# Kernel optimization log

Measured on AMD Instinct MI355X. Metric: run time of the kernel, lower is better.

## Reference

```python
import jax, jax.numpy as jnp
import numpy as np

D_MODEL = 1024
EPS = 1e-6

def setup_inputs() -> dict:
    key = jax.random.key(0)
    ks = jax.random.split(key, 13)
    B, T, S, E = 4, 2048, 2048, D_MODEL
    s = 1.0 / np.sqrt(E)
    return {
        "query": jax.random.normal(ks[0], (B, T, E), jnp.float32),
        "key": jax.random.normal(ks[1], (B, S, E), jnp.float32),
        "value": jax.random.normal(ks[2], (B, S, E), jnp.float32),
        "Wq": jax.random.normal(ks[3], (E, E), jnp.float32) * s,
        "bq": jax.random.normal(ks[4], (E,), jnp.float32) * 0.01,
        "Wk": jax.random.normal(ks[5], (E, E), jnp.float32) * s,
        "bk": jax.random.normal(ks[6], (E,), jnp.float32) * 0.01,
        "Wv": jax.random.normal(ks[7], (E, E), jnp.float32) * s,
        "bv": jax.random.normal(ks[8], (E,), jnp.float32) * 0.01,
        "Wo": jax.random.normal(ks[9], (E, E), jnp.float32) * s,
        "bo": jax.random.normal(ks[10], (E,), jnp.float32) * 0.01,
        "gamma": jnp.ones((E,), jnp.float32),
        "beta": jnp.zeros((E,), jnp.float32),
    }

def reference(query, key, value, Wq, bq, Wk, bk, Wv, bv, Wo, bo, gamma, beta):
    # Note: despite the name, the original never splits heads; attention is
    # over the full d_model with scale 1/sqrt(d_model). Dropout = eval identity.
    residual = query
    q = jnp.einsum('bte,fe->btf', query, Wq) + bq   # nn.Linear: x @ W.T + b
    k = jnp.einsum('bse,fe->bsf', key, Wk) + bk
    v = jnp.einsum('bse,fe->bsf', value, Wv) + bv
    scores = jnp.einsum('bte,bse->bts', q, k) / jnp.sqrt(jnp.float32(D_MODEL))
    attn = jax.nn.softmax(scores, axis=-1)          # (B, T, S)
    ctx = jnp.einsum('bts,bse->bte', attn, v)
    out = jnp.einsum('bte,fe->btf', ctx, Wo) + bo
    out = out + residual
    mu = jnp.mean(out, axis=-1, keepdims=True)
    var = jnp.mean(jnp.square(out - mu), axis=-1, keepdims=True)
    return (out - mu) * jax.lax.rsqrt(var + EPS) * gamma + beta
```

## Files before the change

### kernel.cpp

```cpp
#include <hip/hip_runtime.h>
#include <hip/hip_bf16.h>

typedef __bf16 bf16_t;
typedef __bf16 bf16x4 __attribute__((ext_vector_type(4)));
typedef __bf16 bf16x8 __attribute__((ext_vector_type(8)));
typedef float f32x16 __attribute__((ext_vector_type(16)));

#define E_DIM 1024
#define SEQ   2048
#define NBATCH 4

__global__ __launch_bounds__(256) void k_castw(
    const float* __restrict__ wq, const float* __restrict__ wk,
    const float* __restrict__ wv, const float* __restrict__ wo,
    bf16_t* __restrict__ wqb, bf16_t* __restrict__ wkb,
    bf16_t* __restrict__ wvb, bf16_t* __restrict__ wob) {
  const int b = blockIdx.x;
  const int w = b >> 9, r = b & 511;
  const float* s = (w == 0) ? wq : (w == 1) ? wk : (w == 2) ? wv : wo;
  bf16_t* d = (w == 0) ? wqb : (w == 1) ? wkb : (w == 2) ? wvb : wob;
  const long i = (long)r * 2048 + threadIdx.x * 8;
  const float4 a = *(const float4*)(s + i);
  const float4 c = *(const float4*)(s + i + 4);
  bf16x8 o;
  o[0] = (bf16_t)a.x; o[1] = (bf16_t)a.y; o[2] = (bf16_t)a.z; o[3] = (bf16_t)a.w;
  o[4] = (bf16_t)c.x; o[5] = (bf16_t)c.y; o[6] = (bf16_t)c.z; o[7] = (bf16_t)c.w;
  *(bf16x8*)(d + i) = o;
}

template <int OUTMODE, bool RS, bool AF32>
__global__ __launch_bounds__(256, RS ? 2 : 3) void k_g7(
    const void* __restrict__ Av, int lda, long sA,
    const bf16_t* __restrict__ B, int ldb, long sB,
    void* __restrict__ Cv, int ldc, long sC,
    int K, float scale, const float* __restrict__ bias,
    const float* __restrict__ residual, int GM, int GN) {
  constexpr int ABYTES = AF32 ? 32768 : 16384;
  __shared__ __align__(16) char smem[ABYTES + 16384];

  const int tid  = threadIdx.x;
  const int lane = tid & 63;
  const int wid  = tid >> 6;
  const int wm   = wid >> 1, wn = wid & 1;
  const int hi   = lane >> 5;
  const int l31  = lane & 31;

  const int nwg  = gridDim.x;
  const int orig = blockIdx.x;
  const int wg   = (orig & 7) * (nwg >> 3) + (orig >> 3);
  const int zz   = wg / (GM * GN);
  const int rm   = wg - zz * (GM * GN);
  const int bm   = rm / GN;
  const int bn   = rm - bm * GN;
  const int brow = bm * 128;
  const int bcol = bn * 128;

#define GLL(gaddr, ldsoff)                                                       \
  __builtin_amdgcn_global_load_lds(                                             \
      (const __attribute__((address_space(1))) void*)(gaddr),                   \
      (__attribute__((address_space(3))) void*)(smem + (ldsoff)), 16, 0, 0)

  const float*  A32s = AF32 ? (const float*)Av + zz * sA +
                              (long)(brow + (tid >> 4)) * lda +
                              (((tid & 15) ^ ((tid >> 4) & 15)) << 2)
                            : nullptr;
  const bf16_t* A16s = AF32 ? nullptr
                            : (const bf16_t*)Av + zz * sA +
                              (long)(brow + (tid >> 3)) * lda +
                              (((tid & 7) ^ ((tid >> 3) & 7)) << 3);
  const bf16_t* Bs   = B + zz * sB + (long)(bcol + (tid >> 3)) * ldb +
                       (((tid & 7) ^ ((tid >> 3) & 7)) << 3);
  const int ldsw = wid << 10;

  auto stage = [&](int t) {
    const long koff = (long)t * 64;
    if constexpr (AF32) {
#pragma unroll
      for (int s = 0; s < 8; ++s)
        GLL(A32s + (long)(s * 16) * lda + koff, s * 4096 + ldsw);
    } else {
#pragma unroll
      for (int s = 0; s < 4; ++s)
        GLL(A16s + (long)(s * 32) * lda + koff, s * 4096 + ldsw);
    }
#pragma unroll
    for (int s = 0; s < 4; ++s)
      GLL(Bs + (long)(s * 32) * ldb + koff, ABYTES + s * 4096 + ldsw);
  };

  auto ldA = [&](int kk, int ra) -> bf16x8 {
    if constexpr (AF32) {
      const int b = kk * 64 + (hi << 5);
      const int sw = (ra & 15) << 4;
      const float4 f0 = *(const float4*)(smem + ra * 256 + (b ^ sw));
      const float4 f1 = *(const float4*)(smem + ra * 256 + ((b + 16) ^ sw));
      bf16x8 r;
      r[0] = (bf16_t)f0.x; r[1] = (bf16_t)f0.y; r[2] = (bf16_t)f0.z; r[3] = (bf16_t)f0.w;
      r[4] = (bf16_t)f1.x; r[5] = (bf16_t)f1.y; r[6] = (bf16_t)f1.z; r[7] = (bf16_t)f1.w;
      return r;
    } else {
      const int b = kk * 32 + (hi << 4);
      return *(const bf16x8*)(smem + ra * 128 + (b ^ ((ra & 7) << 4)));
    }
  };
  auto ldB = [&](int kk, int rb) -> bf16x8 {
    const int b = kk * 32 + (hi << 4);
    return *(const bf16x8*)(smem + ABYTES + rb * 128 + (b ^ ((rb & 7) << 4)));
  };

  f32x16 acc00 = {}, acc01 = {}, acc10 = {}, acc11 = {};
  f32x16 rs0 = {}, rs1 = {};
  bf16x8 vones;
#pragma unroll
  for (int i = 0; i < 8; ++i) vones[i] = (bf16_t)1.0f;

  const int ra = wm * 64 + l31;
  const int rb = wn * 64 + l31;
  const int NT = K >> 6;

  for (int t = 0; t < NT; ++t) {
    stage(t);
    __syncthreads();
#pragma unroll
    for (int k = 0; k < 4; ++k) {
      bf16x8 a0 = ldA(k, ra), a1 = ldA(k, ra + 32);
      bf16x8 b0 = ldB(k, rb), b1 = ldB(k, rb + 32);
      acc00 = __builtin_amdgcn_mfma_f32_32x32x16_bf16(a0, b0, acc00, 0, 0, 0);
      acc01 = __builtin_amdgcn_mfma_f32_32x32x16_bf16(a0, b1, acc01, 0, 0, 0);
      acc10 = __builtin_amdgcn_mfma_f32_32x32x16_bf16(a1, b0, acc10, 0, 0, 0);
      acc11 = __builtin_amdgcn_mfma_f32_32x32x16_bf16(a1, b1, acc11, 0, 0, 0);
      if constexpr (RS) {
        rs0 = __builtin_amdgcn_mfma_f32_32x32x16_bf16(a0, vones, rs0, 0, 0, 0);
        rs1 = __builtin_amdgcn_mfma_f32_32x32x16_bf16(a1, vones, rs1, 0, 0, 0);
      }
    }
    __syncthreads();
  }

  float inv0[16], inv1[16];
  if constexpr (RS) {
#pragma unroll
    for (int i = 0; i < 16; ++i) { inv0[i] = 1.0f / rs0[i]; inv1[i] = 1.0f / rs1[i]; }
  }
  const int colb = bcol + wn * 64 + l31;
  const int rowb = brow + wm * 64 + (hi << 2);
#pragma unroll
  for (int mf = 0; mf < 2; ++mf) {
#pragma unroll
    for (int nf = 0; nf < 2; ++nf) {
      const f32x16 av = (mf == 0) ? (nf == 0 ? acc00 : acc01) : (nf == 0 ? acc10 : acc11);
      const int colg = colb + nf * 32;
      float bval = 0.0f;
      if constexpr (OUTMODE != 3) bval = bias ? bias[colg] : 0.0f;
#pragma unroll
      for (int g = 0; g < 4; ++g) {
        const int r0 = rowb + mf * 32 + g * 8;
        if constexpr (OUTMODE == 2) {
          bf16x4 pk;
#pragma unroll
          for (int j = 0; j < 4; ++j) pk[j] = (bf16_t)(av[g * 4 + j] * scale + bval);
          const long bb = (long)(r0 >> 11);
          const int ss = r0 & (SEQ - 1);
          *(bf16x4*)((bf16_t*)Cv + bb * ((long)E_DIM * SEQ) + (long)colg * SEQ + ss) = pk;
        } else {
#pragma unroll
          for (int j = 0; j < 4; ++j) {
            const int r = r0 + j;
            float v;
            if constexpr (OUTMODE == 3) v = __expf(av[g * 4 + j] * scale);
            else v = av[g * 4 + j] * scale + bval;
            if constexpr (RS) v *= (mf == 0 ? inv0[g * 4 + j] : inv1[g * 4 + j]);
            if (OUTMODE == 0 && residual) v += residual[(long)r * ldc + colg];
            const long idx = (long)zz * sC + (long)r * ldc + colg;
            if constexpr (OUTMODE == 0) ((float*)Cv)[idx] = v;
            else ((bf16_t*)Cv)[idx] = (bf16_t)v;
          }
        }
      }
    }
  }
#undef GLL
}

__global__ __launch_bounds__(256) void k_layernorm(float* __restrict__ out,
                                                   const float* __restrict__ gamma,
                                                   const float* __restrict__ beta) {
  const long row = blockIdx.x;
  float* rp = out + row * 1024;
  const int t = threadIdx.x;
  const float4 v = *(const float4*)(rp + t * 4);
  float s = v.x + v.y + v.z + v.w;
#pragma unroll
  for (int o = 32; o; o >>= 1) s += __shfl_xor(s, o);
  __shared__ float red1[4], red2[4];
  const int lane = t & 63, w = t >> 6;
  if (lane == 0) red1[w] = s;
  __syncthreads();
  const float mu = (red1[0] + red1[1] + red1[2] + red1[3]) * (1.0f / 1024.0f);
  const float d0 = v.x - mu, d1 = v.y - mu, d2 = v.z - mu, d3 = v.w - mu;
  float ss = d0 * d0 + d1 * d1 + d2 * d2 + d3 * d3;
#pragma unroll
  for (int o = 32; o; o >>= 1) ss += __shfl_xor(ss, o);
  if (lane == 0) red2[w] = ss;
  __syncthreads();
  const float var = (red2[0] + red2[1] + red2[2] + red2[3]) * (1.0f / 1024.0f);
  const float rsq = rsqrtf(var + 1e-6f);
  const float4 g = *(const float4*)(gamma + t * 4);
  const float4 b = *(const float4*)(beta + t * 4);
  float4 o;
  o.x = d0 * rsq * g.x + b.x;
  o.y = d1 * rsq * g.y + b.y;
  o.z = d2 * rsq * g.z + b.z;
  o.w = d3 * rsq * g.w + b.w;
  *(float4*)(rp + t * 4) = o;
}

extern "C" void kernel_launch(void* const* d_in, const int* in_sizes, int n_in,
                              void* d_out, int out_size, void* d_ws, size_t ws_size,
                              hipStream_t stream) {
  const float* query = (const float*)d_in[0];
  const float* key   = (const float*)d_in[1];
  const float* value = (const float*)d_in[2];
  const float* Wq = (const float*)d_in[3];
  const float* bq = (const float*)d_in[4];
  const float* Wk = (const float*)d_in[5];
  const float* bk = (const float*)d_in[6];
  const float* Wv = (const float*)d_in[7];
  const float* bv = (const float*)d_in[8];
  const float* Wo = (const float*)d_in[9];
  const float* bo = (const float*)d_in[10];
  const float* gamma = (const float*)d_in[11];
  const float* beta  = (const float*)d_in[12];
  float* out = (float*)d_out;

  char* ws = (char*)d_ws;
  const size_t XSZ = (size_t)NBATCH * SEQ * E_DIM * 2;
  const size_t WSZ = (size_t)E_DIM * E_DIM * 2;
  const size_t B2  = 3 * XSZ;

  bf16_t* SC  = (bf16_t*)(ws + 0);
  bf16_t* Wqb = (bf16_t*)(ws + B2);
  bf16_t* Wkb = (bf16_t*)(ws + B2 + WSZ);
  bf16_t* Wvb = (bf16_t*)(ws + B2 + 2 * WSZ);
  bf16_t* Wob = (bf16_t*)(ws + B2 + 3 * WSZ);
  bf16_t* Qb  = (bf16_t*)(ws + B2 + 4 * WSZ);
  bf16_t* Kb  = (bf16_t*)(ws + B2 + 4 * WSZ + XSZ);
  bf16_t* Vt  = (bf16_t*)(ws + B2 + 4 * WSZ + 2 * XSZ);
  bf16_t* Ctx = (bf16_t*)(ws + B2 + 4 * WSZ + 3 * XSZ);

  const int NTOK = NBATCH * SEQ;

  k_castw<<<dim3(2048), 256, 0, stream>>>(Wq, Wk, Wv, Wo, Wqb, Wkb, Wvb, Wob);

  k_g7<1, false, true><<<512, 256, 0, stream>>>(
      query, E_DIM, 0, Wqb, E_DIM, 0, Qb, E_DIM, 0, E_DIM, 1.0f, bq, nullptr, 64, 8);
  k_g7<1, false, true><<<512, 256, 0, stream>>>(
      key, E_DIM, 0, Wkb, E_DIM, 0, Kb, E_DIM, 0, E_DIM, 1.0f, bk, nullptr, 64, 8);
  k_g7<2, false, true><<<512, 256, 0, stream>>>(
      value, E_DIM, 0, Wvb, E_DIM, 0, Vt, 0, 0, E_DIM, 1.0f, bv, nullptr, 64, 8);

  k_g7<3, false, false><<<1024, 256, 0, stream>>>(
      Qb, E_DIM, (long)SEQ * E_DIM, Kb, E_DIM, (long)SEQ * E_DIM,
      SC, SEQ, (long)SEQ * SEQ, E_DIM, 0.03125f, nullptr, nullptr, 16, 16);

  k_g7<1, true, false><<<512, 256, 0, stream>>>(
      SC, SEQ, (long)SEQ * SEQ, Vt, SEQ, (long)E_DIM * SEQ,
      Ctx, E_DIM, (long)SEQ * E_DIM, SEQ, 1.0f, nullptr, nullptr, 16, 8);

  k_g7<0, false, false><<<512, 256, 0, stream>>>(
      Ctx, E_DIM, 0, Wob, E_DIM, 0, out, E_DIM, 0, E_DIM, 1.0f, bo, query, 64, 8);

  k_layernorm<<<dim3(NTOK), 256, 0, stream>>>(out, gamma, beta);
}
```

Before: 258.4 us.

## Triple-buffer GEMM with 128x256 tiles and pre-cast activations to bf16

```diff
diff --git a/kernel.cpp b/kernel.cpp
--- a/kernel.cpp
+++ b/kernel.cpp
@@ -10,16 +10,29 @@
 #define SEQ   2048
 #define NBATCH 4
 
-__global__ __launch_bounds__(256) void k_castw(
+#define BARR()  asm volatile("s_barrier" ::: "memory")
+#define VMC12() asm volatile("s_waitcnt vmcnt(12)" ::: "memory")
+#define VMC0()  asm volatile("s_waitcnt vmcnt(0)" ::: "memory")
+
+__global__ __launch_bounds__(256) void k_cast_all(
+    const float* __restrict__ q, const float* __restrict__ k, const float* __restrict__ v,
     const float* __restrict__ wq, const float* __restrict__ wk,
     const float* __restrict__ wv, const float* __restrict__ wo,
+    bf16_t* __restrict__ xq, bf16_t* __restrict__ xk, bf16_t* __restrict__ xv,
     bf16_t* __restrict__ wqb, bf16_t* __restrict__ wkb,
     bf16_t* __restrict__ wvb, bf16_t* __restrict__ wob) {
   const int b = blockIdx.x;
-  const int w = b >> 9, r = b & 511;
-  const float* s = (w == 0) ? wq : (w == 1) ? wk : (w == 2) ? wv : wo;
-  bf16_t* d = (w == 0) ? wqb : (w == 1) ? wkb : (w == 2) ? wvb : wob;
-  const long i = (long)r * 2048 + threadIdx.x * 8;
+  const float* s; bf16_t* d; long base;
+  if (b < 4096)        { s = q; d = xq; base = (long)b * 2048; }
+  else if (b < 8192)   { s = k; d = xk; base = (long)(b - 4096) * 2048; }
+  else if (b < 12288)  { s = v; d = xv; base = (long)(b - 8192) * 2048; }
+  else {
+    const int w = (b - 12288) >> 9, r = (b - 12288) & 511;
+    s = (w == 0) ? wq : (w == 1) ? wk : (w == 2) ? wv : wo;
+    d = (w == 0) ? wqb : (w == 1) ? wkb : (w == 2) ? wvb : wob;
+    base = (long)r * 2048;
+  }
+  const long i = base + threadIdx.x * 8;
   const float4 a = *(const float4*)(s + i);
   const float4 c = *(const float4*)(s + i + 4);
   bf16x8 o;
@@ -28,20 +41,20 @@
   *(bf16x8*)(d + i) = o;
 }
 
-template <int OUTMODE, bool RS, bool AF32>
-__global__ __launch_bounds__(256, RS ? 2 : 3) void k_g7(
-    const void* __restrict__ Av, int lda, long sA,
+template <int OUTMODE, bool RS>
+__global__ __launch_bounds__(512, 2) void k_g8(
+    const bf16_t* __restrict__ A, int lda, long sA,
     const bf16_t* __restrict__ B, int ldb, long sB,
     void* __restrict__ Cv, int ldc, long sC,
     int K, float scale, const float* __restrict__ bias,
     const float* __restrict__ residual, int GM, int GN) {
-  constexpr int ABYTES = AF32 ? 32768 : 16384;
-  __shared__ __align__(16) char smem[ABYTES + 16384];
+  extern __shared__ char smem[];
 
   const int tid  = threadIdx.x;
   const int lane = tid & 63;
   const int wid  = tid >> 6;
-  const int wm   = wid >> 1, wn = wid & 1;
+  const int wm   = wid >> 2;
+  const int wn   = wid & 3;
   const int hi   = lane >> 5;
   const int l31  = lane & 31;
 
@@ -53,59 +66,29 @@
   const int bm   = rm / GN;
   const int bn   = rm - bm * GN;
   const int brow = bm * 128;
-  const int bcol = bn * 128;
+  const int bcol = bn * 256;
 
 #define GLL(gaddr, ldsoff)                                                       \
   __builtin_amdgcn_global_load_lds(                                             \
       (const __attribute__((address_space(1))) void*)(gaddr),                   \
       (__attribute__((address_space(3))) void*)(smem + (ldsoff)), 16, 0, 0)
 
-  const float*  A32s = AF32 ? (const float*)Av + zz * sA +
-                              (long)(brow + (tid >> 4)) * lda +
-                              (((tid & 15) ^ ((tid >> 4) & 15)) << 2)
-                            : nullptr;
-  const bf16_t* A16s = AF32 ? nullptr
-                            : (const bf16_t*)Av + zz * sA +
-                              (long)(brow + (tid >> 3)) * lda +
-                              (((tid & 7) ^ ((tid >> 3) & 7)) << 3);
-  const bf16_t* Bs   = B + zz * sB + (long)(bcol + (tid >> 3)) * ldb +
-                       (((tid & 7) ^ ((tid >> 3) & 7)) << 3);
+  const int colk = ((tid & 7) ^ ((tid >> 3) & 7)) << 3;
+  const bf16_t* Asrc = A + zz * sA + (long)(brow + (tid >> 3)) * lda + colk;
+  const bf16_t* Bsrc = B + zz * sB + (long)(bcol + (tid >> 3)) * ldb + colk;
   const int ldsw = wid << 10;
 
-  auto stage = [&](int t) {
+  const int NT = K >> 6;
+
+  auto stage = [&](int t, int buf) {
     const long koff = (long)t * 64;
-    if constexpr (AF32) {
-#pragma unroll
-      for (int s = 0; s < 8; ++s)
-        GLL(A32s + (long)(s * 16) * lda + koff, s * 4096 + ldsw);
-    } else {
-#pragma unroll
-      for (int s = 0; s < 4; ++s)
-        GLL(A16s + (long)(s * 32) * lda + koff, s * 4096 + ldsw);
-    }
+    const int bb = buf * 49152;
+#pragma unroll
+    for (int s = 0; s < 2; ++s)
+      GLL(Asrc + (long)(s * 64) * lda + koff, bb + s * 8192 + ldsw);
 #pragma unroll
     for (int s = 0; s < 4; ++s)
-      GLL(Bs + (long)(s * 32) * ldb + koff, ABYTES + s * 4096 + ldsw);
-  };
-
-  auto ldA = [&](int kk, int ra) -> bf16x8 {
-    if constexpr (AF32) {
-      const int b = kk * 64 + (hi << 5);
-      const int sw = (ra & 15) << 4;
-      const float4 f0 = *(const float4*)(smem + ra * 256 + (b ^ sw));
-      const float4 f1 = *(const float4*)(smem + ra * 256 + ((b + 16) ^ sw));
-      bf16x8 r;
-      r[0] = (bf16_t)f0.x; r[1] = (bf16_t)f0.y; r[2] = (bf16_t)f0.z; r[3] = (bf16_t)f0.w;
-      r[4] = (bf16_t)f1.x; r[5] = (bf16_t)f1.y; r[6] = (bf16_t)f1.z; r[7] = (bf16_t)f1.w;
-      return r;
-    } else {
-      const int b = kk * 32 + (hi << 4);
-      return *(const bf16x8*)(smem + ra * 128 + (b ^ ((ra & 7) << 4)));
-    }
-  };
-  auto ldB = [&](int kk, int rb) -> bf16x8 {
-    const int b = kk * 32 + (hi << 4);
-    return *(const bf16x8*)(smem + ABYTES + rb * 128 + (b ^ ((rb & 7) << 4)));
+      GLL(Bsrc + (long)(s * 64) * ldb + koff, bb + 16384 + s * 8192 + ldsw);
   };
 
   f32x16 acc00 = {}, acc01 = {}, acc10 = {}, acc11 = {};
@@ -116,15 +99,25 @@
 
   const int ra = wm * 64 + l31;
   const int rb = wn * 64 + l31;
-  const int NT = K >> 6;
-
-  for (int t = 0; t < NT; ++t) {
-    stage(t);
-    __syncthreads();
-#pragma unroll
-    for (int k = 0; k < 4; ++k) {
-      bf16x8 a0 = ldA(k, ra), a1 = ldA(k, ra + 32);
-      bf16x8 b0 = ldB(k, rb), b1 = ldB(k, rb + 32);
+  const int swzA = (ra & 7) << 4;
+  const int swzB = (rb & 7) << 4;
+
+  stage(0, 0);
+  stage(1 < NT ? 1 : 0, 1);
+
+  for (int T = 0; T < NT; ++T) {
+    BARR();
+    stage(T + 2 < NT ? T + 2 : NT - 1, (T + 2) % 3);
+    VMC12();
+    BARR();
+    const char* bufp = smem + (T % 3) * 49152;
+#pragma unroll
+    for (int kk = 0; kk < 4; ++kk) {
+      const int cb = kk * 32 + (hi << 4);
+      bf16x8 a0 = *(const bf16x8*)(bufp + ra * 128 + (cb ^ swzA));
+      bf16x8 a1 = *(const bf16x8*)(bufp + (ra + 32) * 128 + (cb ^ swzA));
+      bf16x8 b0 = *(const bf16x8*)(bufp + 16384 + rb * 128 + (cb ^ swzB));
+      bf16x8 b1 = *(const bf16x8*)(bufp + 16384 + (rb + 32) * 128 + (cb ^ swzB));
       acc00 = __builtin_amdgcn_mfma_f32_32x32x16_bf16(a0, b0, acc00, 0, 0, 0);
       acc01 = __builtin_amdgcn_mfma_f32_32x32x16_bf16(a0, b1, acc01, 0, 0, 0);
       acc10 = __builtin_amdgcn_mfma_f32_32x32x16_bf16(a1, b0, acc10, 0, 0, 0);
@@ -134,8 +127,8 @@
         rs1 = __builtin_amdgcn_mfma_f32_32x32x16_bf16(a1, vones, rs1, 0, 0, 0);
       }
     }
-    __syncthreads();
-  }
+  }
+  VMC0();
 
   float inv0[16], inv1[16];
   if constexpr (RS) {
@@ -159,9 +152,9 @@
           bf16x4 pk;
 #pragma unroll
           for (int j = 0; j < 4; ++j) pk[j] = (bf16_t)(av[g * 4 + j] * scale + bval);
-          const long bb = (long)(r0 >> 11);
+          const long bb2 = (long)(r0 >> 11);
           const int ss = r0 & (SEQ - 1);
-          *(bf16x4*)((bf16_t*)Cv + bb * ((long)E_DIM * SEQ) + (long)colg * SEQ + ss) = pk;
+          *(bf16x4*)((bf16_t*)Cv + bb2 * ((long)E_DIM * SEQ) + (long)colg * SEQ + ss) = pk;
         } else {
 #pragma unroll
           for (int j = 0; j < 4; ++j) {
@@ -238,6 +231,9 @@
   const size_t WSZ = (size_t)E_DIM * E_DIM * 2;
   const size_t B2  = 3 * XSZ;
 
+  bf16_t* Xq  = (bf16_t*)(ws + 0);
+  bf16_t* Xk  = (bf16_t*)(ws + XSZ);
+  bf16_t* Xv  = (bf16_t*)(ws + 2 * XSZ);
   bf16_t* SC  = (bf16_t*)(ws + 0);
   bf16_t* Wqb = (bf16_t*)(ws + B2);
   bf16_t* Wkb = (bf16_t*)(ws + B2 + WSZ);
@@ -249,26 +245,34 @@
   bf16_t* Ctx = (bf16_t*)(ws + B2 + 4 * WSZ + 3 * XSZ);
 
   const int NTOK = NBATCH * SEQ;
-
-  k_castw<<<dim3(2048), 256, 0, stream>>>(Wq, Wk, Wv, Wo, Wqb, Wkb, Wvb, Wob);
-
-  k_g7<1, false, true><<<512, 256, 0, stream>>>(
-      query, E_DIM, 0, Wqb, E_DIM, 0, Qb, E_DIM, 0, E_DIM, 1.0f, bq, nullptr, 64, 8);
-  k_g7<1, false, true><<<512, 256, 0, stream>>>(
-      key, E_DIM, 0, Wkb, E_DIM, 0, Kb, E_DIM, 0, E_DIM, 1.0f, bk, nullptr, 64, 8);
-  k_g7<2, false, true><<<512, 256, 0, stream>>>(
-      value, E_DIM, 0, Wvb, E_DIM, 0, Vt, 0, 0, E_DIM, 1.0f, bv, nullptr, 64, 8);
-
-  k_g7<3, false, false><<<1024, 256, 0, stream>>>(
+  const int SMB = 147456;
+
+  hipFuncSetAttribute((const void*)k_g8<1, false>, hipFuncAttributeMaxDynamicSharedMemorySize, SMB);
+  hipFuncSetAttribute((const void*)k_g8<2, false>, hipFuncAttributeMaxDynamicSharedMemorySize, SMB);
+  hipFuncSetAttribute((const void*)k_g8<3, false>, hipFuncAttributeMaxDynamicSharedMemorySize, SMB);
+  hipFuncSetAttribute((const void*)k_g8<1, true>,  hipFuncAttributeMaxDynamicSharedMemorySize, SMB);
+  hipFuncSetAttribute((const void*)k_g8<0, false>, hipFuncAttributeMaxDynamicSharedMemorySize, SMB);
+
+  k_cast_all<<<dim3(14336), 256, 0, stream>>>(query, key, value, Wq, Wk, Wv, Wo,
+                                              Xq, Xk, Xv, Wqb, Wkb, Wvb, Wob);
+
+  k_g8<1, false><<<256, 512, SMB, stream>>>(
+      Xq, E_DIM, 0, Wqb, E_DIM, 0, Qb, E_DIM, 0, E_DIM, 1.0f, bq, nullptr, 64, 4);
+  k_g8<1, false><<<256, 512, SMB, stream>>>(
+      Xk, E_DIM, 0, Wkb, E_DIM, 0, Kb, E_DIM, 0, E_DIM, 1.0f, bk, nullptr, 64, 4);
+  k_g8<2, false><<<256, 512, SMB, stream>>>(
+      Xv, E_DIM, 0, Wvb, E_DIM, 0, Vt, 0, 0, E_DIM, 1.0f, bv, nullptr, 64, 4);
+
+  k_g8<3, false><<<512, 512, SMB, stream>>>(
       Qb, E_DIM, (long)SEQ * E_DIM, Kb, E_DIM, (long)SEQ * E_DIM,
-      SC, SEQ, (long)SEQ * SEQ, E_DIM, 0.03125f, nullptr, nullptr, 16, 16);
-
-  k_g7<1, true, false><<<512, 256, 0, stream>>>(
+      SC, SEQ, (long)SEQ * SEQ, E_DIM, 0.03125f, nullptr, nullptr, 16, 8);
+
+  k_g8<1, true><<<256, 512, SMB, stream>>>(
       SC, SEQ, (long)SEQ * SEQ, Vt, SEQ, (long)E_DIM * SEQ,
-      Ctx, E_DIM, (long)SEQ * E_DIM, SEQ, 1.0f, nullptr, nullptr, 16, 8);
-
-  k_g7<0, false, false><<<512, 256, 0, stream>>>(
-      Ctx, E_DIM, 0, Wob, E_DIM, 0, out, E_DIM, 0, E_DIM, 1.0f, bo, query, 64, 8);
+      Ctx, E_DIM, (long)SEQ * E_DIM, SEQ, 1.0f, nullptr, nullptr, 16, 4);
+
+  k_g8<0, false><<<256, 512, SMB, stream>>>(
+      Ctx, E_DIM, 0, Wob, E_DIM, 0, out, E_DIM, 0, E_DIM, 1.0f, bo, query, 64, 4);
 
   k_layernorm<<<dim3(NTOK), 256, 0, stream>>>(out, gamma, beta);
 }
```

Measured after the change: 260.0 us. About the same (+0.6%).
